# Kernel optimization log

Measured on AMD Instinct MI355X. Metric: run time of the kernel, lower is better.

Reference implementation:

```python
import jax, jax.numpy as jnp
import numpy as np

N_HEAD = 12

def setup_inputs() -> dict:
    key = jax.random.key(0)
    k1, k2, k3 = jax.random.split(key, 3)
    B, T, C = 8, 1024, 768
    x = jax.random.normal(k1, (B, T, C), dtype=jnp.float32)
    # torch Linear(768, 3*768): store as [in, out] so we can do x @ W
    W_attn = jax.random.normal(k2, (C, 3 * C), dtype=jnp.float32) * 0.02
    b_attn = jax.random.normal(k3, (3 * C,), dtype=jnp.float32) * 0.02
    return {"x": x, "W_attn": W_attn, "b_attn": b_attn}

def reference(x, W_attn, b_attn):
    B, T, C = x.shape
    H = N_HEAD
    hs = C // H
    scale = 1.0 / jnp.sqrt(jnp.asarray(hs, dtype=x.dtype))
    qkv = x @ W_attn + b_attn                      # [B,T,3C]
    q, k, v = jnp.split(qkv, 3, axis=-1)
    q = q.reshape(B, T, H, hs).transpose(0, 2, 1, 3)  # [B,H,T,hs]
    k = k.reshape(B, T, H, hs).transpose(0, 2, 1, 3)
    v = v.reshape(B, T, H, hs).transpose(0, 2, 1, 3)
    scores = jnp.einsum('bhqd,bhkd->bhqk', q, k) * scale
    # causal mask then ReLU (masked -inf entries become 0 after ReLU)
    causal = jnp.tril(jnp.ones((T, T), dtype=bool))
    att = jnp.where(causal[None, None], jax.nn.relu(scores), jnp.zeros((), dtype=scores.dtype))
    out = jnp.einsum('bhqk,bhkd->bhqd', att, v)    # [B,H,T,hs]
    out = out.transpose(0, 2, 1, 3).reshape(B, T, C)
    return out
```

## Files before the change

kernel.cpp:

```cpp
#include <hip/hip_runtime.h>

typedef __attribute__((ext_vector_type(8))) short bf16x8;
typedef __attribute__((ext_vector_type(4))) float f32x4;
typedef __attribute__((ext_vector_type(4))) unsigned short us4;
typedef __attribute__((ext_vector_type(8))) unsigned short us8;

#define MFMA(a, b, c) __builtin_amdgcn_mfma_f32_16x16x32_bf16((a), (b), (c), 0, 0, 0)

__device__ __forceinline__ unsigned short f2bf(float f) {
  unsigned u = __builtin_bit_cast(unsigned, f);
  u = (u + 0x7fffu + ((u >> 16) & 1u)) >> 16;
  return (unsigned short)u;
}

__device__ __forceinline__ void gload16(const void* g, void* l) {
  __builtin_amdgcn_global_load_lds((const __attribute__((address_space(1))) void*)g,
                                   (__attribute__((address_space(3))) void*)l,
                                   16, 0, 0);
}

__device__ __forceinline__ bf16x8 readfrag(const unsigned short* buf, int row, int kbyte) {
  int byte = row * 128 + kbyte;
  byte ^= (row & 7) << 4;
  return *(const bf16x8*)((const char*)buf + byte);
}

__global__ void cast_x_kernel(const float* __restrict__ x,
                              unsigned short* __restrict__ xb, int n4) {
  int id = blockIdx.x * blockDim.x + threadIdx.x;
  if (id >= n4) return;
  float4 v = ((const float4*)x)[id];
  us4 o = { f2bf(v.x), f2bf(v.y), f2bf(v.z), f2bf(v.w) };
  ((us4*)xb)[id] = o;
}

__global__ void castw_kernel(const float* __restrict__ W,
                             unsigned short* __restrict__ Wt) {
  __shared__ unsigned short tile[32][33];
  int bn = blockIdx.x * 32;
  int bk = blockIdx.y * 32;
  int lx = threadIdx.x & 31, ly = threadIdx.x >> 5;
#pragma unroll
  for (int i = 0; i < 32; i += 8)
    tile[ly + i][lx] = f2bf(W[(bk + ly + i) * 2304 + bn + lx]);
  __syncthreads();
#pragma unroll
  for (int i = 0; i < 32; i += 8)
    Wt[(bn + ly + i) * 768 + bk + lx] = tile[lx][ly + i];
}

__global__ __launch_bounds__(512, 2) void qkv_gemm_kernel(
    const unsigned short* __restrict__ xb, const unsigned short* __restrict__ wt,
    const float* __restrict__ bias,
    unsigned short* __restrict__ qb, unsigned short* __restrict__ kb,
    unsigned short* __restrict__ vb) {
  __shared__ unsigned short lds[65536];
  const int tid = threadIdx.x;
  const int lane = tid & 63, wid = tid >> 6;
  const int wm = wid >> 1, wn = wid & 1;
  const int l15 = lane & 15, lg = lane >> 4;

  int bid = blockIdx.x;
  int xcd = bid & 7, c = bid >> 3;
  int mb = (xcd & 3) * 8 + (c & 7);
  int nb = (xcd >> 2) * 9 + (c >> 3);
  const int m0 = mb * 256, n0 = nb * 128;

  const unsigned short* Ab_g = xb + (size_t)m0 * 768;
  const unsigned short* Bb_g = wt + (size_t)n0 * 768;

  int eA[4], sA[4], eB[2], sB[2];
#pragma unroll
  for (int i = 0; i < 4; ++i) {
    int e = (i * 512 + tid) * 8, row = e >> 6;
    eA[i] = e;
    sA[i] = row * 768 + ((e ^ ((row & 7) << 3)) & 63);
  }
#pragma unroll
  for (int i = 0; i < 2; ++i) {
    int e = (i * 512 + tid) * 8, row = e >> 6;
    eB[i] = e;
    sB[i] = row * 768 + ((e ^ ((row & 7) << 3)) & 63);
  }

#define SA(buf, k0, i) gload16(Ab_g + sA[i] + (k0), &lds[(buf) * 16384 + eA[i]])
#define SB(buf, k0, i) gload16(Bb_g + sB[i] + (k0), &lds[49152 + (buf) * 8192 + eB[i]])

  f32x4 acc[4][4] = {};
  bf16x8 bfr[4][2];

  SA(0, 0, 0); SA(0, 0, 1); SA(0, 0, 2); SA(0, 0, 3);
  SB(0, 0, 0); SB(0, 0, 1);
  SA(1, 64, 0); SA(1, 64, 1); SA(1, 64, 2); SA(1, 64, 3);
  asm volatile("s_waitcnt vmcnt(4)" ::: "memory");
  __builtin_amdgcn_s_barrier();

#define GPHASE(cA_, cB_, Q, STG, EW)                                              \
  {                                                                               \
    const unsigned short* Abuf = &lds[(cA_) * 16384];                             \
    const unsigned short* Bbuf = &lds[49152 + (cB_) * 8192];                      \
    bf16x8 afr[2][2];                                                             \
    _Pragma("unroll") for (int m2 = 0; m2 < 2; ++m2)                              \
        _Pragma("unroll") for (int kk = 0; kk < 2; ++kk)                          \
            afr[m2][kk] =                                                         \
        readfrag(Abuf, wm * 64 + ((Q) * 2 + m2) * 16 + l15, kk * 64 + lg * 16);   \
    if ((Q) == 0) {                                                               \
      _Pragma("unroll") for (int nf = 0; nf < 4; ++nf)                            \
          _Pragma("unroll") for (int kk = 0; kk < 2; ++kk)                        \
              bfr[nf][kk] =                                                       \
          readfrag(Bbuf, wn * 64 + nf * 16 + l15, kk * 64 + lg * 16);             \
    }                                                                             \
    STG;                                                                          \
    __builtin_amdgcn_sched_barrier(0);                                            \
    __builtin_amdgcn_s_barrier();                                                 \
    asm volatile("s_waitcnt lgkmcnt(0)" ::: "memory");                            \
    __builtin_amdgcn_sched_barrier(0);                                            \
    __builtin_amdgcn_s_setprio(1);                                                \
    _Pragma("unroll") for (int m2 = 0; m2 < 2; ++m2)                              \
        _Pragma("unroll") for (int nf = 0; nf < 4; ++nf)                          \
            _Pragma("unroll") for (int kk = 0; kk < 2; ++kk)                      \
                acc[(Q) * 2 + m2][nf] =                                           \
        MFMA(afr[m2][kk], bfr[nf][kk], acc[(Q) * 2 + m2][nf]);                    \
    __builtin_amdgcn_s_setprio(0);                                                \
    EW;                                                                           \
    __builtin_amdgcn_sched_barrier(0);                                            \
    __builtin_amdgcn_s_barrier();                                                 \
  }

  int cA = 0;
  for (int kt = 0; kt < 10; ++kt) {
    int cB = kt & 1, cBn = cB ^ 1;
    int cA2 = cA + 2; if (cA2 >= 3) cA2 -= 3;
    int k1 = (kt + 1) * 64, k2 = (kt + 2) * 64;
    GPHASE(cA, cB, 0,
           { SB(cBn, k1, 0); SB(cBn, k1, 1); SA(cA2, k2, 0); SA(cA2, k2, 1); }, );
    GPHASE(cA, cB, 1, { SA(cA2, k2, 2); SA(cA2, k2, 3); },
           asm volatile("s_waitcnt vmcnt(4)" ::: "memory"));
    cA = (cA == 2) ? 0 : cA + 1;
  }
  GPHASE(cA, 0, 0, { SB(1, 704, 0); SB(1, 704, 1); }, );
  GPHASE(cA, 0, 1, ,
         asm volatile("s_waitcnt vmcnt(0)" ::: "memory"));
  cA = (cA == 2) ? 0 : cA + 1;
  GPHASE(cA, 1, 0, , );
  GPHASE(cA, 1, 1, , );

  __syncthreads();

  const int sec = n0 / 768;
  float bcol[4];
#pragma unroll
  for (int nf = 0; nf < 4; ++nf) bcol[nf] = bias[n0 + wn * 64 + nf * 16 + l15];

  if (sec < 2) {
    unsigned short* ct = lds;
#pragma unroll
    for (int mf = 0; mf < 4; ++mf)
#pragma unroll
      for (int nf = 0; nf < 4; ++nf)
#pragma unroll
        for (int r = 0; r < 4; ++r)
          ct[(wm * 64 + mf * 16 + lg * 4 + r) * 128 + wn * 64 + nf * 16 + l15] =
              f2bf(acc[mf][nf][r] + bcol[nf]);
    __syncthreads();
    unsigned short* dstbase = (sec == 0) ? qb : kb;
    const int hbase = (n0 - sec * 768) >> 6;
    const int g8 = tid >> 3, l8 = tid & 7;
#pragma unroll
    for (int j = 0; j < 8; ++j) {
      int chunk = j * 64 + g8;
      int row = chunk >> 1, hh = chunk & 1;
      us8 v = *(const us8*)&ct[row * 128 + hh * 64 + l8 * 8];
      int t = m0 + row, bb = t >> 10, tt = t & 1023;
      *(us8*)(dstbase + ((size_t)((bb * 12 + hbase + hh) * 1024 + tt)) * 64 + l8 * 8) = v;
    }
  } else {
#pragma unroll
    for (int nf = 0; nf < 4; ++nf) {
      int cc = (n0 - 1536) + wn * 64 + nf * 16 + l15;
      int h = cc >> 6, d = cc & 63;
#pragma unroll
      for (int mf = 0; mf < 4; ++mf) {
        int row0 = m0 + wm * 64 + mf * 16 + lg * 4;
        int bb = row0 >> 10, t0 = row0 & 1023;
        us4 o;
#pragma unroll
        for (int r = 0; r < 4; ++r) o[r] = f2bf(acc[mf][nf][r] + bcol[nf]);
        *(us4*)(vb + ((size_t)((bb * 12 + h) * 64 + d)) * 1024 + t0) = o;
      }
    }
  }
#undef SA
#undef SB
#undef GPHASE
}

__global__ __launch_bounds__(256) void attn_kernel(
    const unsigned short* __restrict__ qb, const unsigned short* __restrict__ kb,
    const unsigned short* __restrict__ vb, float* __restrict__ out) {
  __shared__ unsigned short ldsK[64 * 64];
  __shared__ unsigned short ldsV[64 * 64];
  __shared__ unsigned short ldsS[64 * 72];
  const int tid = threadIdx.x;
  const int lane = tid & 63, wid = tid >> 6;
  const int l15 = lane & 15, lg = lane >> 4;
  const int bh = blockIdx.x;
  const int q0 = blockIdx.y * 64;
  const int b = bh / 12, h = bh % 12;
  const size_t base = (size_t)bh * 65536;

  const unsigned short* qp = qb + base + (size_t)(q0 + wid * 16 + l15) * 64 + lg * 8;
  bf16x8 aq[2];
  aq[0] = *(const bf16x8*)qp;
  aq[1] = *(const bf16x8*)(qp + 32);

  f32x4 o[4] = {};

  const int nkt = (q0 >> 6) + 1;
  for (int kt = 0; kt < nkt; ++kt) {
#pragma unroll
    for (int r = 0; r < 2; ++r) {
      int e = (r * 256 + tid) * 8;
      int row = e >> 6;
      int esw = e ^ ((row & 7) << 3);
      gload16(kb + base + kt * 4096 + esw, &ldsK[e]);
      gload16(vb + base + (size_t)row * 1024 + kt * 64 + (esw & 63), &ldsV[e]);
    }
    __syncthreads();

    f32x4 s[4] = {};
#pragma unroll
    for (int kk = 0; kk < 2; ++kk)
#pragma unroll
      for (int nf = 0; nf < 4; ++nf) {
        bf16x8 bk = readfrag(ldsK, nf * 16 + l15, kk * 64 + lg * 16);
        s[nf] = MFMA(aq[kk], bk, s[nf]);
      }

#pragma unroll
    for (int nf = 0; nf < 4; ++nf) {
      int col = nf * 16 + l15;
      int gk = kt * 64 + col;
#pragma unroll
      for (int r = 0; r < 4; ++r) {
        int qrow = wid * 16 + lg * 4 + r;
        float v = s[nf][r] * 0.125f;
        v = (gk <= q0 + qrow) ? fmaxf(v, 0.0f) : 0.0f;
        ldsS[qrow * 72 + col] = f2bf(v);
      }
    }
    __syncthreads();

#pragma unroll
    for (int kk = 0; kk < 2; ++kk) {
      bf16x8 as = *(const bf16x8*)&ldsS[(wid * 16 + l15) * 72 + kk * 32 + lg * 8];
#pragma unroll
      for (int df = 0; df < 4; ++df) {
        bf16x8 bv = readfrag(ldsV, df * 16 + l15, kk * 64 + lg * 16);
        o[df] = MFMA(as, bv, o[df]);
      }
    }
    __syncthreads();
  }

#pragma unroll
  for (int df = 0; df < 4; ++df) {
    int d = df * 16 + l15;
#pragma unroll
    for (int r = 0; r < 4; ++r) {
      int t = q0 + wid * 16 + lg * 4 + r;
      out[(size_t)(b * 1024 + t) * 768 + h * 64 + d] = o[df][r];
    }
  }
}

extern "C" void kernel_launch(void* const* d_in, const int* in_sizes, int n_in,
                              void* d_out, int out_size, void* d_ws, size_t ws_size,
                              hipStream_t stream) {
  const float* x = (const float*)d_in[0];
  const float* W = (const float*)d_in[1];
  const float* bias = (const float*)d_in[2];
  float* out = (float*)d_out;

  unsigned short* xb = (unsigned short*)d_ws;
  unsigned short* wt = xb + 6291456;
  unsigned short* qb = wt + 1769472;
  unsigned short* kb = qb + 6291456;
  unsigned short* vb = kb + 6291456;

  cast_x_kernel<<<6144, 256, 0, stream>>>(x, xb, 1572864);
  castw_kernel<<<dim3(72, 24), 256, 0, stream>>>(W, wt);
  qkv_gemm_kernel<<<576, 512, 0, stream>>>(xb, wt, bias, qb, kb, vb);
  attn_kernel<<<dim3(96, 16), 256, 0, stream>>>(qb, kb, vb, out);
}
```

Before: 102.7 us.

## Restructure attention kernel with larger Q tiles, split-K waves, and double-buffered K/V

The attention kernel now uses 512-thread blocks, each covering 256 query rows. Each wave owns 64 query rows and half of the key tiles (even or odd), with partial outputs reduced through LDS at the end. K/V tiles are double-buffered in LDS via async global-to-LDS loads, and blocks are mapped to XCDs so heads share cache. The causal mask is applied only on diagonal tiles, and MFMA sections get raised priority. The aim is more reuse per K/V load, fewer barriers and overlapped loads, at the cost of larger register and LDS use and an uneven per-block workload.

Measured after the change: 114.4 us. +11.5%, slower.

```diff
diff --git a/kernel.cpp b/kernel.cpp
--- a/kernel.cpp
+++ b/kernel.cpp
@@ -195,82 +195,143 @@
 #undef GPHASE
 }
 
-__global__ __launch_bounds__(256) void attn_kernel(
+__global__ __launch_bounds__(512) void attn_kernel(
     const unsigned short* __restrict__ qb, const unsigned short* __restrict__ kb,
     const unsigned short* __restrict__ vb, float* __restrict__ out) {
-  __shared__ unsigned short ldsK[64 * 64];
-  __shared__ unsigned short ldsV[64 * 64];
-  __shared__ unsigned short ldsS[64 * 72];
+  __shared__ unsigned short lds[65536];
   const int tid = threadIdx.x;
   const int lane = tid & 63, wid = tid >> 6;
+  const int qs = wid >> 1, ks = wid & 1;
   const int l15 = lane & 15, lg = lane >> 4;
-  const int bh = blockIdx.x;
-  const int q0 = blockIdx.y * 64;
+
+  int bid = blockIdx.x;
+  int xcd = bid & 7, c = bid >> 3;
+  int bh = xcd * 12 + (c % 12);
+  int byq = 3 - (c / 12);
   const int b = bh / 12, h = bh % 12;
   const size_t base = (size_t)bh * 65536;
-
-  const unsigned short* qp = qb + base + (size_t)(q0 + wid * 16 + l15) * 64 + lg * 8;
-  bf16x8 aq[2];
-  aq[0] = *(const bf16x8*)qp;
-  aq[1] = *(const bf16x8*)(qp + 32);
-
-  f32x4 o[4] = {};
-
-  const int nkt = (q0 >> 6) + 1;
-  for (int kt = 0; kt < nkt; ++kt) {
-#pragma unroll
-    for (int r = 0; r < 2; ++r) {
-      int e = (r * 256 + tid) * 8;
-      int row = e >> 6;
-      int esw = e ^ ((row & 7) << 3);
-      gload16(kb + base + kt * 4096 + esw, &ldsK[e]);
-      gload16(vb + base + (size_t)row * 1024 + kt * 64 + (esw & 63), &ldsV[e]);
+  const int Q = byq * 4 + qs;
+  const int qr0 = byq * 256 + qs * 64;
+
+  bf16x8 aq[4][2];
+#pragma unroll
+  for (int mf = 0; mf < 4; ++mf)
+#pragma unroll
+    for (int kk = 0; kk < 2; ++kk)
+      aq[mf][kk] = *(const bf16x8*)(qb + base + (size_t)(qr0 + mf * 16 + l15) * 64 +
+                                    kk * 32 + lg * 8);
+
+  const int e = tid * 8;
+  const int row = e >> 6;
+  const int esw = e ^ ((row & 7) << 3);
+
+#define ASTAGE(buf, i_)                                                            \
+  {                                                                                \
+    int kt0 = 2 * (i_);                                                            \
+    gload16(kb + base + (size_t)kt0 * 4096 + esw, &lds[(buf) * 8192 + e]);         \
+    gload16(kb + base + (size_t)(kt0 + 1) * 4096 + esw,                            \
+            &lds[(buf) * 8192 + 4096 + e]);                                        \
+    gload16(vb + base + (size_t)row * 1024 + kt0 * 64 + (esw & 63),                \
+            &lds[16384 + (buf) * 8192 + e]);                                       \
+    gload16(vb + base + (size_t)row * 1024 + (kt0 + 1) * 64 + (esw & 63),          \
+            &lds[16384 + (buf) * 8192 + 4096 + e]);                                \
+  }
+
+  f32x4 o[4][4] = {};
+  unsigned short* Sb = &lds[32768 + wid * 4096];
+
+  const int niter = 2 * byq + 2;
+  ASTAGE(0, 0);
+  asm volatile("s_waitcnt vmcnt(0)" ::: "memory");
+  __builtin_amdgcn_s_barrier();
+
+  for (int i = 0; i < niter; ++i) {
+    const int cur = i & 1;
+    if (i + 1 < niter) ASTAGE(cur ^ 1, i + 1);
+    const int kt = 2 * i + ks;
+    if (kt <= Q) {
+      const unsigned short* Kb = &lds[cur * 8192 + ks * 4096];
+      const unsigned short* Vb = &lds[16384 + cur * 8192 + ks * 4096];
+      bf16x8 bk[4][2];
+#pragma unroll
+      for (int nf = 0; nf < 4; ++nf)
+#pragma unroll
+        for (int kk = 0; kk < 2; ++kk)
+          bk[nf][kk] = readfrag(Kb, nf * 16 + l15, kk * 64 + lg * 16);
+      f32x4 s[4][4] = {};
+      __builtin_amdgcn_s_setprio(1);
+#pragma unroll
+      for (int mf = 0; mf < 4; ++mf)
+#pragma unroll
+        for (int nf = 0; nf < 4; ++nf)
+#pragma unroll
+          for (int kk = 0; kk < 2; ++kk)
+            s[mf][nf] = MFMA(aq[mf][kk], bk[nf][kk], s[mf][nf]);
+      __builtin_amdgcn_s_setprio(0);
+      const bool diag = (kt == Q);
+#pragma unroll
+      for (int mf = 0; mf < 4; ++mf)
+#pragma unroll
+        for (int nf = 0; nf < 4; ++nf) {
+          int colk = nf * 16 + l15;
+#pragma unroll
+          for (int r = 0; r < 4; ++r) {
+            int rowq = mf * 16 + lg * 4 + r;
+            float v = fmaxf(s[mf][nf][r] * 0.125f, 0.0f);
+            if (diag && colk > rowq) v = 0.0f;
+            int byte = (rowq * 128 + colk * 2) ^ ((rowq & 7) << 4);
+            *(unsigned short*)((char*)Sb + byte) = f2bf(v);
+          }
+        }
+      bf16x8 pa[4][2];
+#pragma unroll
+      for (int mf = 0; mf < 4; ++mf)
+#pragma unroll
+        for (int kk = 0; kk < 2; ++kk)
+          pa[mf][kk] = readfrag(Sb, mf * 16 + l15, kk * 64 + lg * 16);
+      __builtin_amdgcn_s_setprio(1);
+#pragma unroll
+      for (int mf = 0; mf < 4; ++mf)
+#pragma unroll
+        for (int df = 0; df < 4; ++df)
+#pragma unroll
+          for (int kk = 0; kk < 2; ++kk)
+            o[mf][df] = MFMA(pa[mf][kk], readfrag(Vb, df * 16 + l15, kk * 64 + lg * 16),
+                             o[mf][df]);
+      __builtin_amdgcn_s_setprio(0);
     }
-    __syncthreads();
-
-    f32x4 s[4] = {};
-#pragma unroll
-    for (int kk = 0; kk < 2; ++kk)
-#pragma unroll
-      for (int nf = 0; nf < 4; ++nf) {
-        bf16x8 bk = readfrag(ldsK, nf * 16 + l15, kk * 64 + lg * 16);
-        s[nf] = MFMA(aq[kk], bk, s[nf]);
-      }
-
-#pragma unroll
-    for (int nf = 0; nf < 4; ++nf) {
-      int col = nf * 16 + l15;
-      int gk = kt * 64 + col;
-#pragma unroll
-      for (int r = 0; r < 4; ++r) {
-        int qrow = wid * 16 + lg * 4 + r;
-        float v = s[nf][r] * 0.125f;
-        v = (gk <= q0 + qrow) ? fmaxf(v, 0.0f) : 0.0f;
-        ldsS[qrow * 72 + col] = f2bf(v);
-      }
-    }
-    __syncthreads();
-
-#pragma unroll
-    for (int kk = 0; kk < 2; ++kk) {
-      bf16x8 as = *(const bf16x8*)&ldsS[(wid * 16 + l15) * 72 + kk * 32 + lg * 8];
-#pragma unroll
-      for (int df = 0; df < 4; ++df) {
-        bf16x8 bv = readfrag(ldsV, df * 16 + l15, kk * 64 + lg * 16);
-        o[df] = MFMA(as, bv, o[df]);
-      }
-    }
-    __syncthreads();
-  }
-
-#pragma unroll
-  for (int df = 0; df < 4; ++df) {
-    int d = df * 16 + l15;
-#pragma unroll
-    for (int r = 0; r < 4; ++r) {
-      int t = q0 + wid * 16 + lg * 4 + r;
-      out[(size_t)(b * 1024 + t) * 768 + h * 64 + d] = o[df][r];
-    }
+    asm volatile("s_waitcnt vmcnt(0)" ::: "memory");
+    __builtin_amdgcn_sched_barrier(0);
+    __builtin_amdgcn_s_barrier();
+  }
+#undef ASTAGE
+
+  float* fr = (float*)lds;
+  if (ks == 1) {
+#pragma unroll
+    for (int mf = 0; mf < 4; ++mf)
+#pragma unroll
+      for (int df = 0; df < 4; ++df)
+#pragma unroll
+        for (int r = 0; r < 4; ++r) {
+          int rowq = mf * 16 + lg * 4 + r, col = df * 16 + l15;
+          int idx = (qs * 4096 + rowq * 64 + col) ^ ((rowq & 4) << 2);
+          fr[idx] = o[mf][df][r];
+        }
+  }
+  __syncthreads();
+  if (ks == 0) {
+#pragma unroll
+    for (int mf = 0; mf < 4; ++mf)
+#pragma unroll
+      for (int df = 0; df < 4; ++df)
+#pragma unroll
+        for (int r = 0; r < 4; ++r) {
+          int rowq = mf * 16 + lg * 4 + r, col = df * 16 + l15;
+          int idx = (qs * 4096 + rowq * 64 + col) ^ ((rowq & 4) << 2);
+          float v = o[mf][df][r] + fr[idx];
+          out[(size_t)(b * 1024 + qr0 + rowq) * 768 + h * 64 + col] = v;
+        }
   }
 }
 
@@ -291,5 +352,5 @@
   cast_x_kernel<<<6144, 256, 0, stream>>>(x, xb, 1572864);
   castw_kernel<<<dim3(72, 24), 256, 0, stream>>>(W, wt);
   qkv_gemm_kernel<<<576, 512, 0, stream>>>(xb, wt, bias, qb, kb, vb);
-  attn_kernel<<<dim3(96, 16), 256, 0, stream>>>(qb, kb, vb, out);
-}
+  attn_kernel<<<384, 512, 0, stream>>>(qb, kb, vb, out);
+}
```
